# Kernel optimization log

Measured on AMD Instinct MI355X. Metric: run time of the kernel, lower is better.

The kernel has to match this reference:

```python
import jax, jax.numpy as jnp
import numpy as np

NUM_EMBEDDINGS = 4096
EMBEDDING_DIM = 256
COMMITMENT_COST = 0.25
N_TOKENS = 32768


def setup_inputs() -> dict:
    key = jax.random.key(0)
    k1, k2 = jax.random.split(key)
    inputs = jax.random.normal(k1, (N_TOKENS, EMBEDDING_DIM), dtype=jnp.float32)
    # torch init: uniform(-1/K, 1/K)
    lim = 1.0 / NUM_EMBEDDINGS
    weight = jax.random.uniform(k2, (NUM_EMBEDDINGS, EMBEDDING_DIM), dtype=jnp.float32,
                                minval=-lim, maxval=lim)
    return {"inputs": inputs, "weight": weight}


def reference(inputs, weight):
    distances = (jnp.sum(inputs ** 2, axis=1, keepdims=True)
                 + jnp.sum(weight ** 2, axis=1)
                 - 2.0 * jnp.matmul(inputs, weight.T))
    encoding_indices = jnp.argmin(distances, axis=1)                       # [N]
    encodings = jax.nn.one_hot(encoding_indices, NUM_EMBEDDINGS,
                               dtype=jnp.float32)                          # [N, K]
    # gather replaces onehot @ weight (same values)
    quantized = weight[encoding_indices]                                   # [N, D]

    commitment_loss = jnp.mean((jax.lax.stop_gradient(quantized) - inputs) ** 2)
    codebook_loss = jnp.mean((quantized - jax.lax.stop_gradient(inputs)) ** 2)
    loss = codebook_loss + COMMITMENT_COST * commitment_loss

    # straight-through estimator
    quantized_st = inputs + jax.lax.stop_gradient(quantized - inputs)

    avg_probs = jnp.mean(encodings, axis=0)                                # [K]
    perplexity = jnp.exp(-jnp.sum(avg_probs * jnp.log(avg_probs + 1e-10)))

    return (quantized_st, perplexity, encodings, encoding_indices, loss)
```

## Files before the change

### kernel.cpp

```cpp
#include <hip/hip_runtime.h>

#define N_TOK 32768
#define N_EMB 4096
#define DIM 256

typedef short bf16x8 __attribute__((ext_vector_type(8)));
typedef float f32x4 __attribute__((ext_vector_type(4)));
typedef unsigned short us8 __attribute__((ext_vector_type(8)));


static __device__ __forceinline__ unsigned short f2bf(float f) {
    unsigned int u = __float_as_uint(f);
    u = (u + 0x7fffu + ((u >> 16) & 1u)) >> 16;
    return (unsigned short)u;
}

__device__ __forceinline__ float pw128_sq(const float4* a4) {
#pragma clang fp contract(off)
    float4 v0 = a4[0], v1 = a4[1];
    float r0 = v0.x * v0.x, r1 = v0.y * v0.y, r2 = v0.z * v0.z, r3 = v0.w * v0.w;
    float r4 = v1.x * v1.x, r5 = v1.y * v1.y, r6 = v1.z * v1.z, r7 = v1.w * v1.w;
    #pragma unroll
    for (int i = 1; i < 16; ++i) {
        v0 = a4[2 * i]; v1 = a4[2 * i + 1];
        float s;
        s = v0.x * v0.x; r0 += s;
        s = v0.y * v0.y; r1 += s;
        s = v0.z * v0.z; r2 += s;
        s = v0.w * v0.w; r3 += s;
        s = v1.x * v1.x; r4 += s;
        s = v1.y * v1.y; r5 += s;
        s = v1.z * v1.z; r6 += s;
        s = v1.w * v1.w; r7 += s;
    }
    return ((r0 + r1) + (r2 + r3)) + ((r4 + r5) + (r6 + r7));
}

__global__ __launch_bounds__(256) void k_prep_w(const float* __restrict__ w,
                                                unsigned short* __restrict__ Wh,
                                                float* __restrict__ e2_np) {
    const int T = blockIdx.x;
    const int t = threadIdx.x, lane = t & 63, g = t >> 6;
    #pragma unroll
    for (int cc = 0; cc < 2; ++cc) {
        int C = g * 2 + cc;
        int row = T * 16 + (lane & 15);
        int col = C * 32 + (lane >> 4) * 8;
        const float* s = w + (size_t)row * DIM + col;
        us8 h;
        #pragma unroll
        for (int j = 0; j < 8; ++j) h[j] = f2bf(s[j]);
        *(us8*)(Wh + ((size_t)(T * 8 + C) * 64 + lane) * 8) = h;
    }
    if (t < 16) {
        int row = T * 16 + t;
        const float4* a = (const float4*)(w + (size_t)row * DIM);
        float lo = pw128_sq(a);
        float hi = pw128_sq(a + 32);
        e2_np[row] = lo + hi;
    }
}

__global__ __launch_bounds__(256, 4) void k_score_mfma(
        const float* __restrict__ x, const float* __restrict__ w,
        const float* __restrict__ e2_np,
        const unsigned short* __restrict__ Wh,
        float* __restrict__ out_idx, unsigned int* __restrict__ counts,
        float* enc,
        float* __restrict__ outq, float* __restrict__ loss_acc) {
    __shared__ __align__(16) short Abuf[8192];
    __shared__ float x2s[32];
    __shared__ float Tmax[4][32];
    __shared__ unsigned int ccnt[32];
    __shared__ int clist[32][16];
    __shared__ float Red_d[32 * 8];
    __shared__ int   Red_i[32 * 8];
    __shared__ float sred[4];

    const int t = threadIdx.x;
    const int wave = t >> 6, lane = t & 63;
    const int tok0 = blockIdx.x * 32;
    const int q = lane >> 4, c = lane & 15;

    {
        int row = t >> 3, seg = t & 7;
        const float* xr = x + (size_t)(tok0 + row) * DIM + seg * 32;
        int base = ((row >> 4) * 8 + seg) * 64;
        int l16 = row & 15;
        #pragma unroll
        for (int j = 0; j < 4; ++j) {
            float4 a = *(const float4*)(xr + j * 8);
            float4 b = *(const float4*)(xr + j * 8 + 4);
            us8 h;
            h[0] = f2bf(a.x); h[1] = f2bf(a.y); h[2] = f2bf(a.z); h[3] = f2bf(a.w);
            h[4] = f2bf(b.x); h[5] = f2bf(b.y); h[6] = f2bf(b.z); h[7] = f2bf(b.w);
            *(us8*)(Abuf + ((size_t)(base + j * 16 + l16)) * 8) = h;
        }
    }
    if (t < 32) {
        ccnt[t] = 0;
        const float4* a = (const float4*)(x + (size_t)(tok0 + t) * DIM);
        float lo = pw128_sq(a);
        float hi = pw128_sq(a + 32);
        x2s[t] = lo + hi;
    }
    __syncthreads();

    f32x4* ez = enc ? (f32x4*)(enc + (size_t)tok0 * N_EMB) : (f32x4*)0;
    const f32x4 zf4 = {0.f, 0.f, 0.f, 0.f};

    float vmax[8], v2[8];
    #pragma unroll
    for (int s = 0; s < 8; ++s) { vmax[s] = -3.4e38f; v2[s] = -3.4e38f; }
    for (int jt = 0; jt < N_EMB; jt += 256) {
        const int U0 = (jt >> 4) + wave * 4;
        f32x4 acc[2][4] = {};
        #pragma unroll
        for (int C = 0; C < 8; ++C) {
            bf16x8 ah[2], bh[4];
            #pragma unroll
            for (int m = 0; m < 2; ++m)
                ah[m] = *(const bf16x8*)(Abuf + (size_t)(m * 8 + C) * 512 + lane * 8);
            #pragma unroll
            for (int n = 0; n < 4; ++n)
                bh[n] = *(const bf16x8*)(Wh + (((size_t)(U0 + n) * 8 + C) * 64 + lane) * 8);
            #pragma unroll
            for (int m = 0; m < 2; ++m)
                #pragma unroll
                for (int n = 0; n < 4; ++n)
                    acc[m][n] = __builtin_amdgcn_mfma_f32_16x16x32_bf16(ah[m], bh[n], acc[m][n], 0, 0, 0);
        }
        {
            unsigned int idb = ((unsigned int)jt >> 8) << 2;
            #pragma unroll
            for (int m = 0; m < 2; ++m)
                #pragma unroll
                for (int n = 0; n < 4; ++n)
                    #pragma unroll
                    for (int r = 0; r < 4; ++r) {
                        float p = __uint_as_float(
                            (__float_as_uint(acc[m][n][r]) & ~63u) | (idb + (unsigned)n));
                        int s = m * 4 + r;
                        if (p > vmax[s]) { v2[s] = vmax[s]; vmax[s] = p; }
                        else if (p > v2[s]) v2[s] = p;
                    }
        }
        if (ez) {
            int base = (jt >> 8) * 8 * 256 + t;
            #pragma unroll
            for (int j = 0; j < 8; ++j)
                __builtin_nontemporal_store(zf4, ez + base + j * 256);
        }
    }
    float rmax[8];
    #pragma unroll
    for (int s = 0; s < 8; ++s) rmax[s] = vmax[s];
    #pragma unroll
    for (int off = 1; off < 16; off <<= 1)
        #pragma unroll
        for (int s = 0; s < 8; ++s)
            rmax[s] = fmaxf(rmax[s], __shfl_xor(rmax[s], off));
    if (c == 0) {
        #pragma unroll
        for (int m = 0; m < 2; ++m)
            #pragma unroll
            for (int r = 0; r < 4; ++r)
                Tmax[wave][m * 16 + q * 4 + r] = rmax[m * 4 + r];
    }
    __syncthreads();
    if (t < 32) {
        float mx = fmaxf(fmaxf(Tmax[0][t], Tmax[1][t]),
                         fmaxf(Tmax[2][t], Tmax[3][t]));
        Tmax[0][t] = mx - 1.5e-4f;
    }
    __syncthreads();
    float thr[8];
    #pragma unroll
    for (int m = 0; m < 2; ++m)
        #pragma unroll
        for (int r = 0; r < 4; ++r)
            thr[m * 4 + r] = Tmax[0][m * 16 + q * 4 + r];

    #pragma unroll
    for (int s = 0; s < 8; ++s) {
        int m = s >> 2, r = s & 3;
        int tokl = m * 16 + q * 4 + r;
        #pragma unroll
        for (int h = 0; h < 2; ++h) {
            float pv = h ? v2[s] : vmax[s];
            if (pv >= thr[s]) {
                unsigned int id = __float_as_uint(pv) & 63u;
                int code = ((int)(id >> 2) * 16 + wave * 4 + (int)(id & 3u)) * 16 + c;
                unsigned int p = atomicAdd(&ccnt[tokl], 1u);
                if (p < 16) clist[tokl][p] = code;
            }
        }
    }
    __syncthreads();

    {
        int token = t >> 3, slot = t & 7;
        int cnt = (int)ccnt[token]; if (cnt > 16) cnt = 16;
        float bd = 3.4e38f;
        int bi = 0x7fffffff;
        float x2 = x2s[token];
        const float4* xr = (const float4*)(x + (size_t)(tok0 + token) * DIM);
        for (int k = slot; k < cnt; k += 8) {
            int code = clist[token][k];
            const float4* wr = (const float4*)(w + (size_t)code * DIM);
            double dot = 0.0;
            for (int g = 0; g < 64; ++g) {
                float4 xv = xr[g];
                float4 wv = wr[g];
                dot += (double)xv.x * (double)wv.x;
                dot += (double)xv.y * (double)wv.y;
                dot += (double)xv.z * (double)wv.z;
                dot += (double)xv.w * (double)wv.w;
            }
            {
#pragma clang fp contract(off)
                float M  = (float)dot;
                float S  = x2 + e2_np[code];
                float dd = S - 2.0f * M;
                if (dd < bd || (dd == bd && code < bi)) { bd = dd; bi = code; }
            }
        }
        Red_d[token * 8 + slot] = bd;
        Red_i[token * 8 + slot] = bi;
    }
    __syncthreads();
    if (t < 32) {
        float fv = Red_d[t * 8];
        int   fi = Red_i[t * 8];
        #pragma unroll
        for (int k = 1; k < 8; ++k) {
            float v = Red_d[t * 8 + k];
            int  ii = Red_i[t * 8 + k];
            if (v < fv || (v == fv && ii < fi)) { fv = v; fi = ii; }
        }
        out_idx[tok0 + t] = (float)fi;
        atomicAdd(&counts[fi], 1u);
        ccnt[t] = (unsigned int)fi;
    }
    __syncthreads();

    {
        int token = t >> 3, slot = t & 7;
        int fi = (int)ccnt[token];
        if (enc && slot == 0)
            __builtin_nontemporal_store(1.0f, enc + (size_t)(tok0 + token) * N_EMB + fi);
        const f32x4* wr = (const f32x4*)(w + (size_t)fi * DIM);
        const f32x4* xr = (const f32x4*)(x + (size_t)(tok0 + token) * DIM);
        f32x4* oq = (f32x4*)(outq + (size_t)(tok0 + token) * DIM);
        float sse = 0.f;
        #pragma unroll
        for (int g0 = 0; g0 < 8; ++g0) {
            int g = slot * 8 + g0;
            f32x4 qv = wr[g];
            f32x4 xv = xr[g];
            __builtin_nontemporal_store(qv, oq + g);
            float dx = qv.x - xv.x, dy = qv.y - xv.y;
            float dz = qv.z - xv.z, dw = qv.w - xv.w;
            sse += dx * dx + dy * dy + dz * dz + dw * dw;
        }
        #pragma unroll
        for (int off = 32; off > 0; off >>= 1) sse += __shfl_down(sse, off, 64);
        if (lane == 0) sred[wave] = sse;
    }
    __syncthreads();
    if (t == 0)
        atomicAdd(loss_acc, sred[0] + sred[1] + sred[2] + sred[3]);
}

__global__ __launch_bounds__(256) void k_onehot(const float* __restrict__ out_idx,
                                                float* __restrict__ enc) {
    int token = blockIdx.x;
    int idx = (int)out_idx[token];
    float4* row = (float4*)(enc + (size_t)token * N_EMB);
    #pragma unroll
    for (int p = 0; p < 4; ++p) {
        int g = threadIdx.x + 256 * p;
        float4 v = make_float4(0.f, 0.f, 0.f, 0.f);
        int d0 = g * 4;
        if (idx >= d0 && idx < d0 + 4) ((float*)&v)[idx - d0] = 1.0f;
        row[g] = v;
    }
}

__global__ __launch_bounds__(256) void k_final(const unsigned int* __restrict__ counts,
                                               const float* __restrict__ loss_acc,
                                               float* __restrict__ out_perp,
                                               float* __restrict__ out_loss) {
    __shared__ float sred[4];
    int t = threadIdx.x;
    float h = 0.f;
    for (int k = t; k < N_EMB; k += 256) {
        float p = (float)counts[k] * (1.0f / N_TOK);
        h += p * logf(p + 1e-10f);
    }
    #pragma unroll
    for (int off = 32; off > 0; off >>= 1) h += __shfl_down(h, off, 64);
    if ((t & 63) == 0) sred[t >> 6] = h;
    __syncthreads();
    if (t == 0) {
        float s = sred[0] + sred[1] + sred[2] + sred[3];
        *out_perp = expf(-s);
        *out_loss = loss_acc[0] * 1.25f / 8388608.0f;
    }
}

extern "C" void kernel_launch(void* const* d_in, const int* in_sizes, int n_in,
                              void* d_out, int out_size, void* d_ws, size_t ws_size,
                              hipStream_t stream) {
    const float* x = (const float*)d_in[0];
    const float* w = (const float*)d_in[1];
    float* out  = (float*)d_out;
    float* out0 = out;
    float* out1 = out0 + 8388608;
    float* out2 = out1 + 1;
    float* out3 = out2 + 134217728;
    float* out4 = out3 + 32768;

    unsigned int* counts = (unsigned int*)d_ws;
    float* loss_acc = (float*)((char*)d_ws + 16384);
    float* e2_np    = (float*)((char*)d_ws + 16896);

    bool big_ws = ws_size >= (size_t)(20u * 1024u * 1024u);
    unsigned short* Wh;
    float* enc_arg;
    if (big_ws) {
        Wh = (unsigned short*)((char*)d_ws + 17u * 1024u * 1024u);
        enc_arg = out2;
    } else {
        uintptr_t sb = ((uintptr_t)out2 + 255) & ~(uintptr_t)255;
        Wh = (unsigned short*)sb;
        enc_arg = nullptr;
    }

    hipMemsetAsync(d_ws, 0, 16640, stream);
    k_prep_w<<<N_EMB / 16, 256, 0, stream>>>(w, Wh, e2_np);
    k_score_mfma<<<N_TOK / 32, 256, 0, stream>>>(x, w, e2_np, Wh,
                                                 out3, counts, enc_arg,
                                                 out0, loss_acc);
    if (!big_ws)
        k_onehot<<<N_TOK, 256, 0, stream>>>(out3, out2);
    k_final<<<1, 256, 0, stream>>>(counts, loss_acc, out1, out4);
}
```

Baseline: 734.7 us.

## Keep token fragments in registers and double-buffer codebook tiles in LDS

Each wave now holds its 16-token bf16 A fragments in registers instead of reading them from shared memory every step. Codebook tiles of 32 codes are streamed into a double-buffered LDS area with global_load_lds, prefetching the next tile while the current one is multiplied. The work split changes from 4 waves × 64 codes × 32 tokens to 2×2 waves over 16 tokens × 16 codes per step, and the step id is packed into 7 low mantissa bits instead of 6. The cost is a __syncthreads every step across 128 steps, and each step issues only one MFMA chain of 8 per wave, which means less instruction-level parallelism per wave.

```diff
diff --git a/kernel.cpp b/kernel.cpp
--- a/kernel.cpp
+++ b/kernel.cpp
@@ -3,6 +3,7 @@
 #define N_TOK 32768
 #define N_EMB 4096
 #define DIM 256
+#define NSTEP 128
 
 typedef short bf16x8 __attribute__((ext_vector_type(8)));
 typedef float f32x4 __attribute__((ext_vector_type(4)));
@@ -68,9 +69,9 @@
         float* __restrict__ out_idx, unsigned int* __restrict__ counts,
         float* enc,
         float* __restrict__ outq, float* __restrict__ loss_acc) {
-    __shared__ __align__(16) short Abuf[8192];
+    __shared__ __align__(16) short Bbuf[2][8192];
     __shared__ float x2s[32];
-    __shared__ float Tmax[4][32];
+    __shared__ float Tmax[2][32];
     __shared__ unsigned int ccnt[32];
     __shared__ int clist[32][16];
     __shared__ float Red_d[32 * 8];
@@ -81,20 +82,29 @@
     const int wave = t >> 6, lane = t & 63;
     const int tok0 = blockIdx.x * 32;
     const int q = lane >> 4, c = lane & 15;
+    const int mt = wave & 1, nb = wave >> 1;
 
     {
-        int row = t >> 3, seg = t & 7;
-        const float* xr = x + (size_t)(tok0 + row) * DIM + seg * 32;
-        int base = ((row >> 4) * 8 + seg) * 64;
-        int l16 = row & 15;
-        #pragma unroll
-        for (int j = 0; j < 4; ++j) {
-            float4 a = *(const float4*)(xr + j * 8);
-            float4 b = *(const float4*)(xr + j * 8 + 4);
+        const unsigned short* sp = Wh + (size_t)wave * 512 + lane * 8;
+        #pragma unroll
+        for (int k = 0; k < 4; ++k)
+            __builtin_amdgcn_global_load_lds(
+                (const __attribute__((address_space(1))) unsigned int*)(sp + k * 2048),
+                (__attribute__((address_space(3))) unsigned int*)(&Bbuf[0][wave * 512 + k * 2048]),
+                16, 0, 0);
+    }
+
+    bf16x8 ah[8];
+    {
+        const float* xrow = x + (size_t)(tok0 + mt * 16 + c) * DIM + q * 8;
+        #pragma unroll
+        for (int C = 0; C < 8; ++C) {
+            float4 a = *(const float4*)(xrow + C * 32);
+            float4 b = *(const float4*)(xrow + C * 32 + 4);
             us8 h;
             h[0] = f2bf(a.x); h[1] = f2bf(a.y); h[2] = f2bf(a.z); h[3] = f2bf(a.w);
             h[4] = f2bf(b.x); h[5] = f2bf(b.y); h[6] = f2bf(b.z); h[7] = f2bf(b.w);
-            *(us8*)(Abuf + ((size_t)(base + j * 16 + l16)) * 8) = h;
+            ah[C] = *(bf16x8*)&h;
         }
     }
     if (t < 32) {
@@ -109,88 +119,71 @@
     f32x4* ez = enc ? (f32x4*)(enc + (size_t)tok0 * N_EMB) : (f32x4*)0;
     const f32x4 zf4 = {0.f, 0.f, 0.f, 0.f};
 
-    float vmax[8], v2[8];
-    #pragma unroll
-    for (int s = 0; s < 8; ++s) { vmax[s] = -3.4e38f; v2[s] = -3.4e38f; }
-    for (int jt = 0; jt < N_EMB; jt += 256) {
-        const int U0 = (jt >> 4) + wave * 4;
-        f32x4 acc[2][4] = {};
+    float vmax[4], v2[4];
+    #pragma unroll
+    for (int r = 0; r < 4; ++r) { vmax[r] = -3.4e38f; v2[r] = -3.4e38f; }
+    for (int s = 0; s < NSTEP; ++s) {
+        const int cur = s & 1;
+        if (s + 1 < NSTEP) {
+            const unsigned short* sp = Wh + (size_t)(s + 1) * 8192 + wave * 512 + lane * 8;
+            short* dp = &Bbuf[cur ^ 1][wave * 512];
+            #pragma unroll
+            for (int k = 0; k < 4; ++k)
+                __builtin_amdgcn_global_load_lds(
+                    (const __attribute__((address_space(1))) unsigned int*)(sp + k * 2048),
+                    (__attribute__((address_space(3))) unsigned int*)(dp + k * 2048),
+                    16, 0, 0);
+        }
+        if (ez)
+            __builtin_nontemporal_store(zf4, ez + s * 256 + t);
+
+        f32x4 acc = {};
         #pragma unroll
         for (int C = 0; C < 8; ++C) {
-            bf16x8 ah[2], bh[4];
-            #pragma unroll
-            for (int m = 0; m < 2; ++m)
-                ah[m] = *(const bf16x8*)(Abuf + (size_t)(m * 8 + C) * 512 + lane * 8);
-            #pragma unroll
-            for (int n = 0; n < 4; ++n)
-                bh[n] = *(const bf16x8*)(Wh + (((size_t)(U0 + n) * 8 + C) * 64 + lane) * 8);
-            #pragma unroll
-            for (int m = 0; m < 2; ++m)
-                #pragma unroll
-                for (int n = 0; n < 4; ++n)
-                    acc[m][n] = __builtin_amdgcn_mfma_f32_16x16x32_bf16(ah[m], bh[n], acc[m][n], 0, 0, 0);
-        }
-        {
-            unsigned int idb = ((unsigned int)jt >> 8) << 2;
-            #pragma unroll
-            for (int m = 0; m < 2; ++m)
-                #pragma unroll
-                for (int n = 0; n < 4; ++n)
-                    #pragma unroll
-                    for (int r = 0; r < 4; ++r) {
-                        float p = __uint_as_float(
-                            (__float_as_uint(acc[m][n][r]) & ~63u) | (idb + (unsigned)n));
-                        int s = m * 4 + r;
-                        if (p > vmax[s]) { v2[s] = vmax[s]; vmax[s] = p; }
-                        else if (p > v2[s]) v2[s] = p;
-                    }
-        }
-        if (ez) {
-            int base = (jt >> 8) * 8 * 256 + t;
-            #pragma unroll
-            for (int j = 0; j < 8; ++j)
-                __builtin_nontemporal_store(zf4, ez + base + j * 256);
-        }
-    }
-    float rmax[8];
-    #pragma unroll
-    for (int s = 0; s < 8; ++s) rmax[s] = vmax[s];
+            bf16x8 bh = *(const bf16x8*)(&Bbuf[cur][((nb * 8 + C) * 64 + lane) * 8]);
+            acc = __builtin_amdgcn_mfma_f32_16x16x32_bf16(ah[C], bh, acc, 0, 0, 0);
+        }
+        #pragma unroll
+        for (int r = 0; r < 4; ++r) {
+            float p = __uint_as_float(
+                (__float_as_uint(acc[r]) & ~127u) | (unsigned)s);
+            if (p > vmax[r]) { v2[r] = vmax[r]; vmax[r] = p; }
+            else if (p > v2[r]) v2[r] = p;
+        }
+        __syncthreads();
+    }
+
+    float rmax[4];
+    #pragma unroll
+    for (int r = 0; r < 4; ++r) rmax[r] = vmax[r];
     #pragma unroll
     for (int off = 1; off < 16; off <<= 1)
         #pragma unroll
-        for (int s = 0; s < 8; ++s)
-            rmax[s] = fmaxf(rmax[s], __shfl_xor(rmax[s], off));
+        for (int r = 0; r < 4; ++r)
+            rmax[r] = fmaxf(rmax[r], __shfl_xor(rmax[r], off));
     if (c == 0) {
         #pragma unroll
-        for (int m = 0; m < 2; ++m)
-            #pragma unroll
-            for (int r = 0; r < 4; ++r)
-                Tmax[wave][m * 16 + q * 4 + r] = rmax[m * 4 + r];
-    }
-    __syncthreads();
-    if (t < 32) {
-        float mx = fmaxf(fmaxf(Tmax[0][t], Tmax[1][t]),
-                         fmaxf(Tmax[2][t], Tmax[3][t]));
-        Tmax[0][t] = mx - 1.5e-4f;
-    }
-    __syncthreads();
-    float thr[8];
-    #pragma unroll
-    for (int m = 0; m < 2; ++m)
-        #pragma unroll
         for (int r = 0; r < 4; ++r)
-            thr[m * 4 + r] = Tmax[0][m * 16 + q * 4 + r];
-
-    #pragma unroll
-    for (int s = 0; s < 8; ++s) {
-        int m = s >> 2, r = s & 3;
-        int tokl = m * 16 + q * 4 + r;
+            Tmax[nb][mt * 16 + q * 4 + r] = rmax[r];
+    }
+    __syncthreads();
+    if (t < 32)
+        Tmax[0][t] = fmaxf(Tmax[0][t], Tmax[1][t]) - 1.5e-4f;
+    __syncthreads();
+    float thr[4];
+    #pragma unroll
+    for (int r = 0; r < 4; ++r)
+        thr[r] = Tmax[0][mt * 16 + q * 4 + r];
+
+    #pragma unroll
+    for (int r = 0; r < 4; ++r) {
+        int tokl = mt * 16 + q * 4 + r;
         #pragma unroll
         for (int h = 0; h < 2; ++h) {
-            float pv = h ? v2[s] : vmax[s];
-            if (pv >= thr[s]) {
-                unsigned int id = __float_as_uint(pv) & 63u;
-                int code = ((int)(id >> 2) * 16 + wave * 4 + (int)(id & 3u)) * 16 + c;
+            float pv = h ? v2[r] : vmax[r];
+            if (pv >= thr[r]) {
+                int sid = (int)(__float_as_uint(pv) & 127u);
+                int code = sid * 32 + nb * 16 + c;
                 unsigned int p = atomicAdd(&ccnt[tokl], 1u);
                 if (p < 16) clist[tokl][p] = code;
             }
```

Result: faster. 685.8 us (-6.7%).
